# Kernel tuning notes

Hardware: AMD Instinct MI355X
Metric: run time of the kernel (lower is better)

The kernel has to match this reference:

```python
import jax, jax.numpy as jnp
import numpy as np

N = 100000      # nodes
E = 1600000     # edges
D_IN = 128      # input_dim
H = 256         # hidden_dim
L = 3           # num_layers
B = 64          # graphs per batch
BN_EPS = 1e-5


def setup_inputs() -> dict:
    key = jax.random.key(0)
    ks = jax.random.split(key, 8)
    x = jax.random.normal(ks[0], (N, D_IN), dtype=jnp.float32)
    edge_index = jax.random.randint(ks[1], (2, E), 0, N, dtype=jnp.int32)
    batch = jnp.sort(jax.random.randint(ks[2], (N,), 0, B, dtype=jnp.int32))
    W0 = jax.random.normal(ks[3], (D_IN, H), dtype=jnp.float32) / np.sqrt(D_IN)
    W_rest = jax.random.normal(ks[4], (L - 1, H, H), dtype=jnp.float32) / np.sqrt(H)
    b = jax.random.normal(ks[5], (L, H), dtype=jnp.float32) * 0.01
    gamma = 1.0 + jax.random.normal(ks[6], (L, H), dtype=jnp.float32) * 0.01
    beta = jax.random.normal(ks[7], (L, H), dtype=jnp.float32) * 0.01
    return {"x": x, "W0": W0, "W_rest": W_rest, "b": b, "gamma": gamma,
            "beta": beta, "edge_index": edge_index, "batch": batch}


def reference(x, W0, W_rest, b, gamma, beta, edge_index, batch):
    src, dst = edge_index[0], edge_index[1]
    # GCN symmetric normalization with self-loops: deg = in-degree + 1
    deg = jax.ops.segment_sum(jnp.ones((E,), x.dtype), dst, num_segments=N) + 1.0
    dis = jax.lax.rsqrt(deg)                   # deg^{-1/2}, [N]
    enorm = dis[src] * dis[dst]                # per-edge norm, [E]
    self_norm = (dis * dis)[:, None]           # self-loop norm = 1/deg, [N,1]

    def gcn_bn_relu(h, W, bb, g, be):
        h = h @ W                                                  # [N,H]
        agg = jax.ops.segment_sum(h[src] * enorm[:, None], dst, num_segments=N)
        h = agg + h * self_norm + bb                               # self-loop + bias
        # BatchNorm1d (training mode: batch stats, biased variance)
        m = h.mean(axis=0)
        v = h.var(axis=0)
        h = (h - m) * jax.lax.rsqrt(v + BN_EPS) * g + be
        return jax.nn.relu(h)                                      # dropout = identity (eval)

    h = gcn_bn_relu(x, W0, b[0], gamma[0], beta[0])
    for i in range(L - 1):
        h = gcn_bn_relu(h, W_rest[i], b[i + 1], gamma[i + 1], beta[i + 1])

    # segment pooling per graph (att_pool in the original is dead code: not returned)
    counts = jax.ops.segment_sum(jnp.ones((N,), h.dtype), batch, num_segments=B)
    mean_pool = jax.ops.segment_sum(h, batch, num_segments=B) / counts[:, None]
    max_pool = jax.ops.segment_max(h, batch, num_segments=B)
    return jnp.concatenate([mean_pool, max_pool], axis=1)          # [B, 2H]
```

## Files before the change

kernel.cpp:

```cpp
#include <hip/hip_runtime.h>
#include <hip/hip_bf16.h>
#include <stdint.h>


#define NN 100000
#define EE 1600000
#define BB 64
#define MPAD 100096
#define NBM (MPAD / 256)

typedef __attribute__((ext_vector_type(8))) short short8;
typedef __attribute__((ext_vector_type(4))) float f32x4;

__device__ __forceinline__ float bflo(uint32_t v){ return __uint_as_float(v << 16); }
__device__ __forceinline__ float bfhi(uint32_t v){ return __uint_as_float(v & 0xffff0000u); }
__device__ __forceinline__ uint32_t bfrne(float x){
  uint32_t u = __float_as_uint(x);
  return (u + 0x7fffu + ((u >> 16) & 1u)) >> 16;
}
__device__ __forceinline__ uint32_t bfpack(float a, float b){ return bfrne(a) | (bfrne(b) << 16); }
__device__ __forceinline__ float phi(long long p){
  return __uint_as_float((uint32_t)((unsigned long long)p >> 32));
}
__device__ __forceinline__ float bnr(float y, float sc, float sh){
  float t = fmaxf(y * sc + sh, 0.f);
  return __uint_as_float(bfrne(t) << 16);
}

__device__ __forceinline__ void gload_lds16(const void* g, void* l){
  __builtin_amdgcn_global_load_lds(
      (const __attribute__((address_space(1))) uint32_t*)g,
      (__attribute__((address_space(3))) uint32_t*)l, 16, 0, 0);
}

__global__ void k_deg(const int* __restrict__ dst, int* __restrict__ degi){
  for (int e = blockIdx.x * blockDim.x + threadIdx.x; e < EE; e += gridDim.x * blockDim.x)
    atomicAdd(&degi[dst[e]], 1);
}

__global__ void k_scan1(const int* __restrict__ degi, int* __restrict__ rp, int* __restrict__ bsum,
                        float* __restrict__ dis){
  __shared__ int lds[256];
  int b = blockIdx.x, t = threadIdx.x;
  int base = b * 1024 + t * 4;
  int v0 = (base + 0 < NN) ? degi[base + 0] : 0;
  int v1 = (base + 1 < NN) ? degi[base + 1] : 0;
  int v2 = (base + 2 < NN) ? degi[base + 2] : 0;
  int v3 = (base + 3 < NN) ? degi[base + 3] : 0;
  if (base + 0 < NN) dis[base + 0] = rsqrtf((float)v0 + 1.0f);
  if (base + 1 < NN) dis[base + 1] = rsqrtf((float)v1 + 1.0f);
  if (base + 2 < NN) dis[base + 2] = rsqrtf((float)v2 + 1.0f);
  if (base + 3 < NN) dis[base + 3] = rsqrtf((float)v3 + 1.0f);
  int s = v0 + v1 + v2 + v3;
  lds[t] = s; __syncthreads();
  for (int off = 1; off < 256; off <<= 1){
    int x = (t >= off) ? lds[t - off] : 0; __syncthreads();
    lds[t] += x; __syncthreads();
  }
  int excl = lds[t] - s;
  if (t == 255) bsum[b] = lds[255];
  if (base + 0 < NN) rp[base + 0] = excl;
  if (base + 1 < NN) rp[base + 1] = excl + v0;
  if (base + 2 < NN) rp[base + 2] = excl + v0 + v1;
  if (base + 3 < NN) rp[base + 3] = excl + v0 + v1 + v2;
}

__global__ void k_scan3(int* __restrict__ rp, int* __restrict__ cursor, const int* __restrict__ bsum){
  __shared__ int red[256];
  int b = blockIdx.x, t = threadIdx.x;
  red[t] = (t < b && t < 98) ? bsum[t] : 0;
  __syncthreads();
  for (int off = 128; off > 0; off >>= 1){
    if (t < off) red[t] += red[t + off];
    __syncthreads();
  }
  int add = red[0];
  int base = b * 1024 + t * 4;
  #pragma unroll
  for (int j = 0; j < 4; ++j){
    int i = base + j;
    if (i < NN){ int v = rp[i] + add; rp[i] = v; cursor[i] = v; }
  }
  if (b == 0 && t == 0) rp[NN] = EE;
}

__global__ void k_fill(const int* __restrict__ src, const int* __restrict__ dst,
                       const float* __restrict__ dis, int* __restrict__ cursor,
                       long long* __restrict__ cp){
  for (int e = blockIdx.x * blockDim.x + threadIdx.x; e < EE; e += gridDim.x * blockDim.x){
    int s = src[e], d = dst[e];
    int pos = atomicAdd(&cursor[d], 1);
    float nrm = dis[s] * dis[d];
    long long v = (long long)(unsigned int)s | ((long long)(unsigned int)__float_as_uint(nrm) << 32);
    cp[pos] = v;
  }
}

__global__ void k_sort(const int* __restrict__ rp, long long* __restrict__ cp){
  int wid = (blockIdx.x * blockDim.x + threadIdx.x) >> 6;
  int lane = threadIdx.x & 63;
  if (wid >= NN) return;
  int beg = rp[wid], end = rp[wid + 1];
  int d = end - beg;
  if (d <= 1) return;
  if (d <= 64){
    long long key = (lane < d) ? cp[beg + lane] : 0x7fffffffffffffffLL;
    #pragma unroll
    for (int k = 2; k <= 64; k <<= 1){
      #pragma unroll
      for (int j = k >> 1; j > 0; j >>= 1){
        long long other = __shfl_xor(key, j);
        bool up = ((lane & k) == 0);
        bool keepMin = (((lane & j) == 0) == up);
        bool take = keepMin ? (other < key) : (other > key);
        if (take) key = other;
      }
    }
    if (lane < d) cp[beg + lane] = key;
  } else if (lane == 0){
    for (int i = beg + 1; i < end; ++i){
      long long k2 = cp[i];
      int j = i - 1;
      while (j >= beg && cp[j] > k2){ cp[j + 1] = cp[j]; --j; }
      cp[j + 1] = k2;
    }
  }
}

__global__ void k_prep(const float* __restrict__ W0, const float* __restrict__ Wr,
                       uint16_t* __restrict__ Wt0, uint16_t* __restrict__ Wt1,
                       uint16_t* __restrict__ Wt2,
                       const float* __restrict__ x, uint32_t* __restrict__ Xb){
  int b = blockIdx.x;
  if (b < 640){
    int i = b * 256 + threadIdx.x;
    if (i < 32768){
      int c = i >> 7, k = i & 127;
      Wt0[i] = (uint16_t)bfrne(W0[k * 256 + c]);
    } else if (i < 32768 + 131072){
      int j = i - 32768;
      int m = j >> 16, jj = j & 65535;
      int c = jj >> 8, k = jj & 255;
      uint16_t v = (uint16_t)bfrne(Wr[m * 65536 + k * 256 + c]);
      if (m == 0) Wt1[jj] = v; else Wt2[jj] = v;
    }
  } else {
    int i = (b - 640) * 256 + threadIdx.x;
    if (i >= MPAD * 64) return;
    int row = i >> 6;
    uint32_t r = 0u;
    if (row < NN){
      int col = (i & 63) * 2;
      r = bfpack(x[row * 128 + col], x[row * 128 + col + 1]);
    }
    Xb[i] = r;
  }
}

__global__ void k_agg256(const uint2* __restrict__ Yin, const int* __restrict__ rp,
                         const long long* __restrict__ cp, const float* __restrict__ dis,
                         const float* __restrict__ ss, uint2* __restrict__ Xout){
  int lane = threadIdx.x & 63;
  int slot = threadIdx.x >> 6;
  float sc0 = ss[lane*4+0], sc1 = ss[lane*4+1], sc2 = ss[lane*4+2], sc3 = ss[lane*4+3];
  float sh0 = ss[256+lane*4+0], sh1 = ss[256+lane*4+1], sh2 = ss[256+lane*4+2], sh3 = ss[256+lane*4+3];
  int row0 = blockIdx.x * 16 + slot;
  for (int rr = 0; rr < 4; ++rr){
    int row = row0 + rr * 4;
    if (row >= NN){
      if (row < MPAD)
        __builtin_nontemporal_store(0ull, (unsigned long long*)&Xout[(size_t)row * 64 + lane]);
      continue;
    }
    int beg = rp[row], end = rp[row + 1];
    float a0 = 0.f, a1 = 0.f, a2 = 0.f, a3 = 0.f;
    int e = beg;
    for (; e + 8 <= end; e += 8){
      long long p[8]; uint2 v[8];
      #pragma unroll
      for (int u = 0; u < 8; ++u) p[u] = cp[e + u];
      #pragma unroll
      for (int u = 0; u < 8; ++u) v[u] = Yin[(size_t)(int)p[u] * 64 + lane];
      #pragma unroll
      for (int u = 0; u < 8; ++u){
        float w = phi(p[u]);
        a0 += w * bnr(bflo(v[u].x), sc0, sh0);
        a1 += w * bnr(bfhi(v[u].x), sc1, sh1);
        a2 += w * bnr(bflo(v[u].y), sc2, sh2);
        a3 += w * bnr(bfhi(v[u].y), sc3, sh3);
      }
    }
    for (; e < end; ++e){
      long long p0 = cp[e];
      float w = phi(p0);
      uint2 v = Yin[(size_t)(int)p0 * 64 + lane];
      a0 += w * bnr(bflo(v.x), sc0, sh0);
      a1 += w * bnr(bfhi(v.x), sc1, sh1);
      a2 += w * bnr(bflo(v.y), sc2, sh2);
      a3 += w * bnr(bfhi(v.y), sc3, sh3);
    }
    float dv = dis[row]; float sn = dv * dv;
    uint2 vs = Yin[(size_t)row * 64 + lane];
    a0 += sn * bnr(bflo(vs.x), sc0, sh0);
    a1 += sn * bnr(bfhi(vs.x), sc1, sh1);
    a2 += sn * bnr(bflo(vs.y), sc2, sh2);
    a3 += sn * bnr(bfhi(vs.y), sc3, sh3);
    unsigned long long o = (unsigned long long)bfpack(a0, a1)
                         | ((unsigned long long)bfpack(a2, a3) << 32);
    __builtin_nontemporal_store(o, (unsigned long long*)&Xout[(size_t)row * 64 + lane]);
  }
}

__global__ void k_agg128(const uint2* __restrict__ Xin, const int* __restrict__ rp,
                         const long long* __restrict__ cp, const float* __restrict__ dis,
                         uint2* __restrict__ Xout){
  int lane = threadIdx.x & 63;
  int half = lane >> 5, j = lane & 31;
  int slot = threadIdx.x >> 6;
  int row0 = blockIdx.x * 16 + slot;
  for (int rr = 0; rr < 4; ++rr){
    int row = row0 + rr * 4;
    if (row >= NN){
      if (row < MPAD && half == 0)
        __builtin_nontemporal_store(0ull, (unsigned long long*)&Xout[(size_t)row * 32 + j]);
      continue;
    }
    int beg = rp[row], end = rp[row + 1];
    float a0 = 0.f, a1 = 0.f, a2 = 0.f, a3 = 0.f;
    int e = beg;
    for (; e + 8 <= end; e += 8){
      long long p[4]; uint2 v[4];
      #pragma unroll
      for (int u = 0; u < 4; ++u) p[u] = cp[e + u * 2 + half];
      #pragma unroll
      for (int u = 0; u < 4; ++u) v[u] = Xin[(size_t)(int)p[u] * 32 + j];
      #pragma unroll
      for (int u = 0; u < 4; ++u){
        float w = phi(p[u]);
        a0 += w * bflo(v[u].x); a1 += w * bfhi(v[u].x);
        a2 += w * bflo(v[u].y); a3 += w * bfhi(v[u].y);
      }
    }
    for (; e < end; e += 2){
      int idx = e + half;
      bool ok = idx < end;
      long long p0 = cp[ok ? idx : end - 1];
      float w = ok ? phi(p0) : 0.f;
      uint2 v = Xin[(size_t)(int)p0 * 32 + j];
      a0 += w * bflo(v.x); a1 += w * bfhi(v.x);
      a2 += w * bflo(v.y); a3 += w * bfhi(v.y);
    }
    a0 += __shfl_xor(a0, 32); a1 += __shfl_xor(a1, 32);
    a2 += __shfl_xor(a2, 32); a3 += __shfl_xor(a3, 32);
    if (half == 0){
      float dv = dis[row]; float sn = dv * dv;
      uint2 vs = Xin[(size_t)row * 32 + j];
      a0 += sn * bflo(vs.x); a1 += sn * bfhi(vs.x);
      a2 += sn * bflo(vs.y); a3 += sn * bfhi(vs.y);
      unsigned long long o = (unsigned long long)bfpack(a0, a1)
                           | ((unsigned long long)bfpack(a2, a3) << 32);
      __builtin_nontemporal_store(o, (unsigned long long*)&Xout[(size_t)row * 32 + j]);
    }
  }
}

template<int K>
__global__ __launch_bounds__(512) void k_gemm(const uint16_t* __restrict__ A,
                                              const uint16_t* __restrict__ Bt,
                                              uint32_t* __restrict__ Cb,
                                              float* __restrict__ pstat){
  __shared__ __align__(16) uint16_t lA[2][8192];
  __shared__ __align__(16) uint16_t lB[2][4096];
  __shared__ float lp[8][128];
  int tid = threadIdx.x;
  int l = tid & 63;
  int bm = blockIdx.x, bn = blockIdx.y;

  f32x4 acc[4][4];
  #pragma unroll
  for (int m = 0; m < 4; ++m)
    #pragma unroll
    for (int n = 0; n < 4; ++n){ f32x4 z = {0.f,0.f,0.f,0.f}; acc[m][n] = z; }

  int w = tid >> 6, wr = w >> 1, wc = w & 1;
  int rbase = wr * 64, cbase = wc * 64;
  int lrow = l & 15, lk8 = l >> 4;

  auto stage = [&](int kt, int buf){
    #pragma unroll
    for (int i = 0; i < 2; ++i){
      int c = i * 512 + tid;
      int k8 = c >> 8, r = c & 255;
      size_t ga = (size_t)(bm * 256 + r) * K + kt * 32 + k8 * 8;
      gload_lds16((const char*)(A + ga), (char*)&lA[buf][c * 8]);
    }
    int k8b = tid >> 7, rb = tid & 127;
    size_t gb = (size_t)(bn * 128 + rb) * K + kt * 32 + k8b * 8;
    gload_lds16((const char*)(Bt + gb), (char*)&lB[buf][tid * 8]);
  };

  stage(0, 0);
  __syncthreads();
  constexpr int NT = K / 32;
  for (int kt = 0; kt < NT; ++kt){
    int cur = kt & 1;
    if (kt + 1 < NT) stage(kt + 1, cur ^ 1);
    short8 afr[4], bfr[4];
    #pragma unroll
    for (int m = 0; m < 4; ++m)
      afr[m] = *(const short8*)&lA[cur][(lk8 * 256 + rbase + m * 16 + lrow) * 8];
    #pragma unroll
    for (int n = 0; n < 4; ++n)
      bfr[n] = *(const short8*)&lB[cur][(lk8 * 128 + cbase + n * 16 + lrow) * 8];
    #pragma unroll
    for (int m = 0; m < 4; ++m)
      #pragma unroll
      for (int n = 0; n < 4; ++n)
        acc[m][n] = __builtin_amdgcn_mfma_f32_16x16x32_bf16(afr[m], bfr[n], acc[m][n], 0, 0, 0);
    __syncthreads();
  }

  int grow0 = bm * 256 + rbase + (l >> 4) * 4;
  int gcol0 = bn * 128 + cbase + (l & 15);
  uint16_t* C16 = (uint16_t*)Cb;
  float sa[4] = {0.f,0.f,0.f,0.f}, sb[4] = {0.f,0.f,0.f,0.f};
  #pragma unroll
  for (int m = 0; m < 4; ++m){
    #pragma unroll
    for (int n = 0; n < 4; ++n){
      int col = gcol0 + n * 16;
      int r0 = grow0 + m * 16;
      f32x4 v = acc[m][n];
      #pragma unroll
      for (int q = 0; q < 4; ++q){
        C16[(size_t)(r0 + q) * 256 + col] = (uint16_t)bfrne(v[q]);
        sa[n] += v[q]; sb[n] += v[q] * v[q];
      }
    }
  }
  #pragma unroll
  for (int n = 0; n < 4; ++n){
    sa[n] += __shfl_xor(sa[n], 16); sa[n] += __shfl_xor(sa[n], 32);
    sb[n] += __shfl_xor(sb[n], 16); sb[n] += __shfl_xor(sb[n], 32);
  }
  if (l < 16){
    #pragma unroll
    for (int n = 0; n < 4; ++n){
      lp[w][n * 16 + l] = sa[n];
      lp[w][64 + n * 16 + l] = sb[n];
    }
  }
  __syncthreads();
  if (tid < 256){
    int kind = tid >> 7, c = tid & 127;
    int wc2 = c >> 6, cc = c & 63;
    float v = lp[wc2][kind * 64 + cc] + lp[2 + wc2][kind * 64 + cc]
            + lp[4 + wc2][kind * 64 + cc] + lp[6 + wc2][kind * 64 + cc];
    pstat[(size_t)(bm * 2 + bn) * 256 + kind * 128 + c] = v;
  }
}

__global__ void k_finalize(const float* __restrict__ pstat, const float* __restrict__ gamma,
                           const float* __restrict__ beta, float* __restrict__ ss){
  int c = threadIdx.x;
  int bn = c >> 7, lc = c & 127;
  double s[8], s2[8];
  #pragma unroll
  for (int j = 0; j < 8; ++j){ s[j] = 0.; s2[j] = 0.; }
  int bm = 0;
  for (; bm + 8 <= NBM; bm += 8){
    #pragma unroll
    for (int j = 0; j < 8; ++j){
      const float* p = pstat + (size_t)((bm + j) * 2 + bn) * 256;
      s[j]  += (double)p[lc];
      s2[j] += (double)p[128 + lc];
    }
  }
  for (; bm < NBM; ++bm){
    const float* p = pstat + (size_t)(bm * 2 + bn) * 256;
    s[0]  += (double)p[lc];
    s2[0] += (double)p[128 + lc];
  }
  double S  = ((s[0]+s[1])+(s[2]+s[3]))  + ((s[4]+s[5])+(s[6]+s[7]));
  double S2 = ((s2[0]+s2[1])+(s2[2]+s2[3])) + ((s2[4]+s2[5])+(s2[6]+s2[7]));
  double mean = S / (double)NN;
  double var  = S2 / (double)NN - mean * mean;
  float rstd = rsqrtf((float)var + 1e-5f);
  float sc = gamma[c] * rstd;
  ss[c] = sc;
  ss[256 + c] = beta[c] - (float)mean * sc;
}

__device__ __forceinline__ int segfind(const int* __restrict__ batch, int g){
  if (g <= 0) return 0;
  if (g >= BB) return NN;
  int lo = 0, hi = NN;
  while (lo < hi){ int mid = (lo + hi) >> 1; if (batch[mid] < g) lo = mid + 1; else hi = mid; }
  return lo;
}

__global__ void k_poolpart(const uint32_t* __restrict__ Y, const float* __restrict__ ss,
                           const int* __restrict__ batch, float* __restrict__ pb){
  int g = blockIdx.x, c = blockIdx.y, t = threadIdx.x;
  float sc0 = ss[2*t], sc1 = ss[2*t+1];
  float sh0 = ss[256+2*t], sh1 = ss[256+2*t+1];
  int s = segfind(batch, g), e = segfind(batch, g + 1);
  int len = e - s;
  int c0 = s + (int)(((long long)len * c) >> 3);
  int c1 = s + (int)(((long long)len * (c + 1)) >> 3);
  float sm0 = 0.f, sm1 = 0.f, mx0 = -1e30f, mx1 = -1e30f;
  #pragma unroll 4
  for (int r = c0; r < c1; ++r){
    uint32_t v = Y[(size_t)r * 128 + t];
    float a  = fmaxf(bflo(v) * sc0 + sh0, 0.f);
    float b2 = fmaxf(bfhi(v) * sc1 + sh1, 0.f);
    sm0 += a; sm1 += b2;
    mx0 = fmaxf(mx0, a); mx1 = fmaxf(mx1, b2);
  }
  float* p = pb + (size_t)(g * 8 + c) * 512;
  p[2 * t] = sm0; p[2 * t + 1] = sm1;
  p[256 + 2 * t] = mx0; p[256 + 2 * t + 1] = mx1;
}

__global__ void k_poolred(const float* __restrict__ pb, const int* __restrict__ batch,
                          float* __restrict__ out){
  int g = blockIdx.x, cc = threadIdx.x;
  float s = 0.f, m = -1e30f;
  #pragma unroll
  for (int c = 0; c < 8; ++c){
    const float* p = pb + (size_t)(g * 8 + c) * 512;
    s += p[cc];
    m = fmaxf(m, p[256 + cc]);
  }
  float inv = 1.0f / (float)(segfind(batch, g + 1) - segfind(batch, g));
  out[g * 512 + cc] = s * inv;
  out[g * 512 + 256 + cc] = m;
}

extern "C" void kernel_launch(void* const* d_in, const int* in_sizes, int n_in,
                              void* d_out, int out_size, void* d_ws, size_t ws_size,
                              hipStream_t stream){
  const float* x     = (const float*)d_in[0];
  const float* W0    = (const float*)d_in[1];
  const float* Wr    = (const float*)d_in[2];
  const float* gamma = (const float*)d_in[4];
  const float* beta  = (const float*)d_in[5];
  const int*   ei    = (const int*)d_in[6];
  const int*   batch = (const int*)d_in[7];
  const int* esrc = ei;
  const int* edst = ei + EE;
  float* out = (float*)d_out;

  char* base = (char*)d_ws;
  size_t off = 0;
  auto alloc = [&](size_t b)->char*{
    char* p = base + off; off = (off + b + 255) & ~(size_t)255; return p;
  };
  uint32_t* Xbuf = (uint32_t*)alloc((size_t)MPAD * 128 * 2);
  uint32_t* Xagg = (uint32_t*)alloc((size_t)MPAD * 256 * 2);
  uint32_t* Y1   = (uint32_t*)alloc((size_t)MPAD * 256 * 2);
  uint32_t* Y2   = (uint32_t*)alloc((size_t)MPAD * 256 * 2);
  uint16_t* Wt0  = (uint16_t*)alloc(256 * 128 * 2);
  uint16_t* Wt1  = (uint16_t*)alloc(256 * 256 * 2);
  uint16_t* Wt2  = (uint16_t*)alloc(256 * 256 * 2);
  int*   degi   = (int*)  alloc((size_t)NN * 4);
  float* dis    = (float*)alloc((size_t)NN * 4);
  int*   rp     = (int*)  alloc((size_t)(NN + 1) * 4);
  int*   cursor = (int*)  alloc((size_t)NN * 4);
  int*   bsum   = (int*)  alloc(128 * 4);
  long long* cp = (long long*)alloc((size_t)EE * 8);
  float* pstat  = (float*)alloc((size_t)NBM * 2 * 256 * 4);
  float* ss     = (float*)alloc(512 * 4);
  float* pb     = (float*)alloc((size_t)BB * 8 * 512 * 4);

  hipMemsetAsync(degi, 0, (size_t)NN * 4, stream);
  k_deg<<<2048, 256, 0, stream>>>(edst, degi);
  k_scan1<<<98, 256, 0, stream>>>(degi, rp, bsum, dis);
  k_scan3<<<98, 256, 0, stream>>>(rp, cursor, bsum);
  k_fill<<<2048, 256, 0, stream>>>(esrc, edst, dis, cursor, cp);
  k_sort<<<NN / 4, 256, 0, stream>>>(rp, cp);
  k_prep<<<640 + MPAD * 64 / 256, 256, 0, stream>>>(W0, Wr, Wt0, Wt1, Wt2, x, Xbuf);

  k_agg128<<<MPAD / 16, 256, 0, stream>>>((const uint2*)Xbuf, rp, cp, dis, (uint2*)Xagg);
  k_gemm<128><<<dim3(NBM, 2), 512, 0, stream>>>((const uint16_t*)Xagg, Wt0, Y1, pstat);
  k_finalize<<<1, 256, 0, stream>>>(pstat, gamma + 0, beta + 0, ss);

  k_agg256<<<MPAD / 16, 256, 0, stream>>>((const uint2*)Y1, rp, cp, dis, ss, (uint2*)Xagg);
  k_gemm<256><<<dim3(NBM, 2), 512, 0, stream>>>((const uint16_t*)Xagg, Wt1, Y2, pstat);
  k_finalize<<<1, 256, 0, stream>>>(pstat, gamma + 256, beta + 256, ss);

  k_agg256<<<MPAD / 16, 256, 0, stream>>>((const uint2*)Y2, rp, cp, dis, ss, (uint2*)Xagg);
  k_gemm<256><<<dim3(NBM, 2), 512, 0, stream>>>((const uint16_t*)Xagg, Wt2, Y1, pstat);
  k_finalize<<<1, 256, 0, stream>>>(pstat, gamma + 512, beta + 512, ss);

  k_poolpart<<<dim3(BB, 8), 128, 0, stream>>>(Y1, ss, batch, pb);
  k_poolred<<<BB, 256, 0, stream>>>(pb, batch, out);
}
```

Before: 772.5 us.

## Fuse BatchNorm finalize into GEMM via last-block atomic counter; vectorize input conversion

Removes the three single-block k_finalize launches. Each GEMM block now bumps an atomic counter after writing its partial statistics, and the last block to finish reduces all partials into the scale/shift buffer. The counters are zeroed by extending the existing degree memset. The x-to-bf16 prep kernel also now converts eight floats per thread with 16-byte loads and stores instead of two scalars. This saves launch gaps and a serial tail, but the final reduction still runs on a single block and adds fences and an atomic to every GEMM block.

After: 1.394 ms. 1.8x slower.

```diff
diff --git a/kernel.cpp b/kernel.cpp
--- a/kernel.cpp
+++ b/kernel.cpp
@@ -130,10 +130,10 @@
 __global__ void k_prep(const float* __restrict__ W0, const float* __restrict__ Wr,
                        uint16_t* __restrict__ Wt0, uint16_t* __restrict__ Wt1,
                        uint16_t* __restrict__ Wt2,
-                       const float* __restrict__ x, uint32_t* __restrict__ Xb){
-  int b = blockIdx.x;
+                       const float* __restrict__ x, uint4* __restrict__ Xb){
+  int b = blockIdx.x, t = threadIdx.x;
   if (b < 640){
-    int i = b * 256 + threadIdx.x;
+    int i = b * 256 + t;
     if (i < 32768){
       int c = i >> 7, k = i & 127;
       Wt0[i] = (uint16_t)bfrne(W0[k * 256 + c]);
@@ -145,15 +145,17 @@
       if (m == 0) Wt1[jj] = v; else Wt2[jj] = v;
     }
   } else {
-    int i = (b - 640) * 256 + threadIdx.x;
-    if (i >= MPAD * 64) return;
-    int row = i >> 6;
-    uint32_t r = 0u;
+    int i = (b - 640) * 256 + t;
+    if (i >= MPAD * 16) return;
+    int row = i >> 4, c8 = i & 15;
+    uint4 o = {0u, 0u, 0u, 0u};
     if (row < NN){
-      int col = (i & 63) * 2;
-      r = bfpack(x[row * 128 + col], x[row * 128 + col + 1]);
-    }
-    Xb[i] = r;
+      const f32x4* xp = (const f32x4*)(x + (size_t)row * 128 + c8 * 8);
+      f32x4 v0 = xp[0], v1 = xp[1];
+      o.x = bfpack(v0[0], v0[1]); o.y = bfpack(v0[2], v0[3]);
+      o.z = bfpack(v1[0], v1[1]); o.w = bfpack(v1[2], v1[3]);
+    }
+    Xb[i] = o;
   }
 }
 
@@ -268,10 +270,15 @@
 __global__ __launch_bounds__(512) void k_gemm(const uint16_t* __restrict__ A,
                                               const uint16_t* __restrict__ Bt,
                                               uint32_t* __restrict__ Cb,
-                                              float* __restrict__ pstat){
+                                              float* __restrict__ pstat,
+                                              const float* __restrict__ gamma,
+                                              const float* __restrict__ beta,
+                                              float* __restrict__ ss,
+                                              int* __restrict__ cnt){
   __shared__ __align__(16) uint16_t lA[2][8192];
   __shared__ __align__(16) uint16_t lB[2][4096];
   __shared__ float lp[8][128];
+  __shared__ int lastflag;
   int tid = threadIdx.x;
   int l = tid & 63;
   int bm = blockIdx.x, bn = blockIdx.y;
@@ -358,37 +365,45 @@
             + lp[4 + wc2][kind * 64 + cc] + lp[6 + wc2][kind * 64 + cc];
     pstat[(size_t)(bm * 2 + bn) * 256 + kind * 128 + c] = v;
   }
-}
-
-__global__ void k_finalize(const float* __restrict__ pstat, const float* __restrict__ gamma,
-                           const float* __restrict__ beta, float* __restrict__ ss){
-  int c = threadIdx.x;
-  int bn = c >> 7, lc = c & 127;
-  double s[8], s2[8];
-  #pragma unroll
-  for (int j = 0; j < 8; ++j){ s[j] = 0.; s2[j] = 0.; }
-  int bm = 0;
-  for (; bm + 8 <= NBM; bm += 8){
-    #pragma unroll
-    for (int j = 0; j < 8; ++j){
-      const float* p = pstat + (size_t)((bm + j) * 2 + bn) * 256;
-      s[j]  += (double)p[lc];
-      s2[j] += (double)p[128 + lc];
-    }
-  }
-  for (; bm < NBM; ++bm){
-    const float* p = pstat + (size_t)(bm * 2 + bn) * 256;
-    s[0]  += (double)p[lc];
-    s2[0] += (double)p[128 + lc];
-  }
-  double S  = ((s[0]+s[1])+(s[2]+s[3]))  + ((s[4]+s[5])+(s[6]+s[7]));
-  double S2 = ((s2[0]+s2[1])+(s2[2]+s2[3])) + ((s2[4]+s2[5])+(s2[6]+s2[7]));
-  double mean = S / (double)NN;
-  double var  = S2 / (double)NN - mean * mean;
-  float rstd = rsqrtf((float)var + 1e-5f);
-  float sc = gamma[c] * rstd;
-  ss[c] = sc;
-  ss[256 + c] = beta[c] - (float)mean * sc;
+
+  __threadfence();
+  __syncthreads();
+  if (tid == 0){
+    int v = atomicAdd(cnt, 1);
+    lastflag = (v == NBM * 2 - 1);
+  }
+  __syncthreads();
+  if (!lastflag) return;
+  __threadfence();
+  if (tid < 256){
+    int c = tid;
+    int bnn = c >> 7, lc = c & 127;
+    double s[8], s2[8];
+    #pragma unroll
+    for (int j2 = 0; j2 < 8; ++j2){ s[j2] = 0.; s2[j2] = 0.; }
+    int b2 = 0;
+    for (; b2 + 8 <= NBM; b2 += 8){
+      #pragma unroll
+      for (int j2 = 0; j2 < 8; ++j2){
+        const float* p = pstat + (size_t)((b2 + j2) * 2 + bnn) * 256;
+        s[j2]  += (double)p[lc];
+        s2[j2] += (double)p[128 + lc];
+      }
+    }
+    for (; b2 < NBM; ++b2){
+      const float* p = pstat + (size_t)(b2 * 2 + bnn) * 256;
+      s[0]  += (double)p[lc];
+      s2[0] += (double)p[128 + lc];
+    }
+    double S  = ((s[0]+s[1])+(s[2]+s[3]))  + ((s[4]+s[5])+(s[6]+s[7]));
+    double S2 = ((s2[0]+s2[1])+(s2[2]+s2[3])) + ((s2[4]+s2[5])+(s2[6]+s2[7]));
+    double mean = S / (double)NN;
+    double var  = S2 / (double)NN - mean * mean;
+    float rstd = rsqrtf((float)var + 1e-5f);
+    float sc = gamma[c] * rstd;
+    ss[c] = sc;
+    ss[256 + c] = beta[c] - (float)mean * sc;
+  }
 }
 
 __device__ __forceinline__ int segfind(const int* __restrict__ batch, int g){
@@ -463,7 +478,9 @@
   uint16_t* Wt0  = (uint16_t*)alloc(256 * 128 * 2);
   uint16_t* Wt1  = (uint16_t*)alloc(256 * 256 * 2);
   uint16_t* Wt2  = (uint16_t*)alloc(256 * 256 * 2);
-  int*   degi   = (int*)  alloc((size_t)NN * 4);
+  int*   zerorg = (int*)  alloc((size_t)(NN + 8) * 4);
+  int*   degi   = zerorg;
+  int*   cnt    = zerorg + NN;
   float* dis    = (float*)alloc((size_t)NN * 4);
   int*   rp     = (int*)  alloc((size_t)(NN + 1) * 4);
   int*   cursor = (int*)  alloc((size_t)NN * 4);
@@ -473,25 +490,25 @@
   float* ss     = (float*)alloc(512 * 4);
   float* pb     = (float*)alloc((size_t)BB * 8 * 512 * 4);
 
-  hipMemsetAsync(degi, 0, (size_t)NN * 4, stream);
+  hipMemsetAsync(zerorg, 0, (size_t)(NN + 8) * 4, stream);
   k_deg<<<2048, 256, 0, stream>>>(edst, degi);
   k_scan1<<<98, 256, 0, stream>>>(degi, rp, bsum, dis);
   k_scan3<<<98, 256, 0, stream>>>(rp, cursor, bsum);
   k_fill<<<2048, 256, 0, stream>>>(esrc, edst, dis, cursor, cp);
   k_sort<<<NN / 4, 256, 0, stream>>>(rp, cp);
-  k_prep<<<640 + MPAD * 64 / 256, 256, 0, stream>>>(W0, Wr, Wt0, Wt1, Wt2, x, Xbuf);
+  k_prep<<<640 + MPAD * 16 / 256, 256, 0, stream>>>(W0, Wr, Wt0, Wt1, Wt2, x, (uint4*)Xbuf);
 
   k_agg128<<<MPAD / 16, 256, 0, stream>>>((const uint2*)Xbuf, rp, cp, dis, (uint2*)Xagg);
-  k_gemm<128><<<dim3(NBM, 2), 512, 0, stream>>>((const uint16_t*)Xagg, Wt0, Y1, pstat);
-  k_finalize<<<1, 256, 0, stream>>>(pstat, gamma + 0, beta + 0, ss);
+  k_gemm<128><<<dim3(NBM, 2), 512, 0, stream>>>((const uint16_t*)Xagg, Wt0, Y1, pstat,
+                                                gamma + 0, beta + 0, ss, cnt + 0);
 
   k_agg256<<<MPAD / 16, 256, 0, stream>>>((const uint2*)Y1, rp, cp, dis, ss, (uint2*)Xagg);
-  k_gemm<256><<<dim3(NBM, 2), 512, 0, stream>>>((const uint16_t*)Xagg, Wt1, Y2, pstat);
-  k_finalize<<<1, 256, 0, stream>>>(pstat, gamma + 256, beta + 256, ss);
+  k_gemm<256><<<dim3(NBM, 2), 512, 0, stream>>>((const uint16_t*)Xagg, Wt1, Y2, pstat,
+                                                gamma + 256, beta + 256, ss, cnt + 1);
 
   k_agg256<<<MPAD / 16, 256, 0, stream>>>((const uint2*)Y2, rp, cp, dis, ss, (uint2*)Xagg);
-  k_gemm<256><<<dim3(NBM, 2), 512, 0, stream>>>((const uint16_t*)Xagg, Wt2, Y1, pstat);
-  k_finalize<<<1, 256, 0, stream>>>(pstat, gamma + 512, beta + 512, ss);
+  k_gemm<256><<<dim3(NBM, 2), 512, 0, stream>>>((const uint16_t*)Xagg, Wt2, Y1, pstat,
+                                                gamma + 512, beta + 512, ss, cnt + 2);
 
   k_poolpart<<<dim3(BB, 8), 128, 0, stream>>>(Y1, ss, batch, pb);
   k_poolred<<<BB, 256, 0, stream>>>(pb, batch, out);
```
